# Performance work log

Measured on AMD Instinct MI355X. Metric: run time of the kernel, lower is better.

## Reference

```python
import jax, jax.numpy as jnp
import numpy as np

B, N, K, D = 256, 64, 12, 128


def setup_inputs() -> dict:
    key = jax.random.key(0)
    ks = jax.random.split(key, 12)
    s = 1.0 / np.sqrt(D)
    inp = {
        "nodes_hidden": jax.random.normal(ks[0], (B, N, D), jnp.float32),
        "neighbors_hidden": jax.random.normal(ks[1], (B, N, K, D), jnp.float32),
        # binary neighbor-validity mask (float, as in the torch code)
        "mask": (jax.random.uniform(ks[2], (B, N, K)) < 0.7).astype(jnp.float32),
        "Wq": jax.random.uniform(ks[3], (D, D), jnp.float32, -s, s),
        "bq": jax.random.uniform(ks[4], (D,), jnp.float32, -s, s),
        "Wk": jax.random.uniform(ks[5], (D, D), jnp.float32, -s, s),
        "bk": jax.random.uniform(ks[6], (D,), jnp.float32, -s, s),
        "Wv": jax.random.uniform(ks[7], (D, D), jnp.float32, -s, s),
        "bv": jax.random.uniform(ks[8], (D,), jnp.float32, -s, s),
        # W_att: Linear(2D -> 1); split into the query half and key half of its weight
        "wa_q": jax.random.uniform(ks[9], (D,), jnp.float32, -s, s),
        "wa_k": jax.random.uniform(ks[10], (D,), jnp.float32, -s, s),
        "ba": jax.random.uniform(ks[11], (), jnp.float32, -s, s),
    }
    return inp


def reference(nodes_hidden, neighbors_hidden, mask, Wq, bq, Wk, bk, Wv, bv, wa_q, wa_k, ba):
    # prepend the node itself to its neighbor list: [B,N,K+1,D]
    nh = jnp.concatenate([nodes_hidden[:, :, None, :], neighbors_hidden], axis=2)
    # prepend an always-valid slot to the mask: [B,N,K+1]
    m = jnp.concatenate([jnp.ones(mask.shape[:-1] + (1,), mask.dtype), mask], axis=-1)

    q = nodes_hidden @ Wq + bq            # [B,N,D]
    k = nh @ Wk + bk                      # [B,N,K+1,D]
    v = nh @ Wv + bv                      # [B,N,K+1,D]

    # W_att(cat([q,k])) == q.wa_q + k.wa_k + ba  (avoids materializing the 2D concat)
    sim = (q @ wa_q)[:, :, None] + k @ wa_k + ba   # [B,N,K+1]
    sim = jnp.where(sim >= 0, sim, 0.2 * sim)      # LeakyReLU(0.2)
    sim = jnp.exp(sim) * m                         # masked exp (matches torch exactly)
    attn = sim / (jnp.sum(sim, axis=-1, keepdims=True) + 1e-16)
    return jnp.einsum('bnk,bnkd->bnd', attn, v)    # [B,N,D]
```

## Files before the change

### kernel.cpp

```cpp
#include <hip/hip_runtime.h>


#define B_  256
#define N_  64
#define K_  12
#define D_  128
#define BN  (B_ * N_)
#define ROWS 8
#define NBLK (BN / ROWS)
#define HB_STRIDE 132

__global__ void __launch_bounds__(256)
fused_kernel(const float* __restrict__ nodes, const float* __restrict__ neigh,
             const float* __restrict__ mask,
             const float* __restrict__ Wq, const float* __restrict__ bq,
             const float* __restrict__ Wk, const float* __restrict__ bk,
             const float* __restrict__ Wv, const float* __restrict__ bv,
             const float* __restrict__ wa_q, const float* __restrict__ wa_k,
             const float* __restrict__ ba_p, float* __restrict__ out) {
    __shared__ float weff[256];
    __shared__ float hb[ROWS * HB_STRIDE];
    __shared__ float scL[ROWS];
    __shared__ float cstS;

    const int t    = threadIdx.x;
    const int wave = t >> 6;
    const int l    = t & 63;

    {
        const float*  wrow = (t < 128) ? (Wq + (size_t)t * D_) : (Wk + (size_t)(t - 128) * D_);
        const float*  wa   = (t < 128) ? wa_q : wa_k;
        const float4* wr4  = (const float4*)wrow;
        const float4* wa4  = (const float4*)wa;
        float acc = 0.0f;
        #pragma unroll
        for (int k = 0; k < 32; ++k) {
            float4 a = wr4[k], b = wa4[k];
            acc += a.x * b.x + a.y * b.y + a.z * b.z + a.w * b.w;
        }
        weff[t] = acc;
    }
    if (wave == 0) {
        float2 q2  = ((const float2*)bq)[l];
        float2 k2  = ((const float2*)bk)[l];
        float2 aq2 = ((const float2*)wa_q)[l];
        float2 ak2 = ((const float2*)wa_k)[l];
        float c = q2.x * aq2.x + q2.y * aq2.y + k2.x * ak2.x + k2.y * ak2.y;
        #pragma unroll
        for (int m = 1; m < 64; m <<= 1) c += __shfl_xor(c, m, 64);
        if (l == 0) cstS = c + ba_p[0];
    }
    __syncthreads();

    const float cst = cstS;
    const float2 wqe = ((const float2*)weff)[l];
    const float2 wke = ((const float2*)(weff + 128))[l];

    #pragma unroll
    for (int p = 0; p < 2; ++p) {
        const int lrow = wave * 2 + p;
        const int idx  = blockIdx.x * ROWS + lrow;

        const float2* np = (const float2*)(nodes + (size_t)idx * D_);
        const float2* gp = (const float2*)(neigh + (size_t)idx * K_ * D_);

        float2 x[K_ + 1];
        x[0] = np[l];
        #pragma unroll
        for (int j = 0; j < K_; ++j) x[j + 1] = gp[j * 64 + l];

        float mval = (l < K_) ? mask[(size_t)idx * K_ + l] : 0.0f;

        float pq = x[0].x * wqe.x + x[0].y * wqe.y;
        float pk[K_ + 1];
        #pragma unroll
        for (int j = 0; j <= K_; ++j) pk[j] = x[j].x * wke.x + x[j].y * wke.y;

        #pragma unroll
        for (int m = 1; m < 64; m <<= 1) {
            pq += __shfl_xor(pq, m, 64);
            #pragma unroll
            for (int j = 0; j <= K_; ++j) pk[j] += __shfl_xor(pk[j], m, 64);
        }

        const float base = pq + cst;
        float e[K_ + 1];
        float S = 0.0f;
        #pragma unroll
        for (int j = 0; j <= K_; ++j) {
            float s = base + pk[j];
            s = (s >= 0.0f) ? s : 0.2f * s;
            float mj = (j == 0) ? 1.0f : __shfl(mval, j - 1, 64);
            e[j] = __expf(s) * mj;
            S += e[j];
        }
        const float inv = 1.0f / (S + 1e-16f);

        float h0 = 0.0f, h1 = 0.0f;
        #pragma unroll
        for (int j = 0; j <= K_; ++j) {
            float w = e[j] * inv;
            h0 += w * x[j].x;
            h1 += w * x[j].y;
        }

        *(float2*)(hb + lrow * HB_STRIDE + 2 * l) = make_float2(h0, h1);
        if (l == 0) scL[lrow] = S * inv;
    }
    __syncthreads();

    const int row  = t >> 5;
    const int cg   = t & 31;
    const int row0 = blockIdx.x * ROWS;
    const float4* wv4 = (const float4*)Wv;

    float4 acc = make_float4(0.f, 0.f, 0.f, 0.f);
    #pragma unroll 8
    for (int k = 0; k < D_; ++k) {
        float4 b = wv4[k * 32 + cg];
        float  a = hb[row * HB_STRIDE + k];
        acc.x += a * b.x;
        acc.y += a * b.y;
        acc.z += a * b.z;
        acc.w += a * b.w;
    }

    float4 bvv = ((const float4*)bv)[cg];
    float  s   = scL[row];
    float4 o;
    o.x = acc.x + bvv.x * s;
    o.y = acc.y + bvv.y * s;
    o.z = acc.z + bvv.z * s;
    o.w = acc.w + bvv.w * s;
    *(float4*)(out + (size_t)(row0 + row) * D_ + cg * 4) = o;
}

extern "C" void kernel_launch(void* const* d_in, const int* in_sizes, int n_in,
                              void* d_out, int out_size, void* d_ws, size_t ws_size,
                              hipStream_t stream) {
    const float* nodes = (const float*)d_in[0];
    const float* neigh = (const float*)d_in[1];
    const float* mask  = (const float*)d_in[2];
    const float* Wq    = (const float*)d_in[3];
    const float* bq    = (const float*)d_in[4];
    const float* Wk    = (const float*)d_in[5];
    const float* bk    = (const float*)d_in[6];
    const float* Wv    = (const float*)d_in[7];
    const float* bv    = (const float*)d_in[8];
    const float* wa_q  = (const float*)d_in[9];
    const float* wa_k  = (const float*)d_in[10];
    const float* ba    = (const float*)d_in[11];
    float* out = (float*)d_out;

    fused_kernel<<<NBLK, 256, 0, stream>>>(nodes, neigh, mask, Wq, bq, Wk, bk,
                                           Wv, bv, wa_q, wa_k, ba, out);
}
```

Measured before the change: 224.8 us.

## Double rows per block, software-pipeline row loads, coalesce weff precompute

Each block now handles 16 rows instead of 8, which halves the number of blocks. The per-block Wq/Wk·wa precompute and the Wv reads in the output GEMV are therefore amortized over twice as many rows. Row loads are double-buffered so the next row's neighbor data is fetched while the current row is processed. The weff precompute now uses coalesced float2 reads with wave reductions instead of strided per-thread row reads. The costs are higher register pressure, fewer blocks for occupancy, and 64 serial shuffle reductions per wave in the precompute.

```diff
diff --git a/kernel.cpp b/kernel.cpp
--- a/kernel.cpp
+++ b/kernel.cpp
@@ -6,7 +6,7 @@
 #define K_  12
 #define D_  128
 #define BN  (B_ * N_)
-#define ROWS 8
+#define ROWS 16
 #define NBLK (BN / ROWS)
 #define HB_STRIDE 132
 
@@ -28,17 +28,20 @@
     const int l    = t & 63;
 
     {
-        const float*  wrow = (t < 128) ? (Wq + (size_t)t * D_) : (Wk + (size_t)(t - 128) * D_);
-        const float*  wa   = (t < 128) ? wa_q : wa_k;
-        const float4* wr4  = (const float4*)wrow;
-        const float4* wa4  = (const float4*)wa;
-        float acc = 0.0f;
-        #pragma unroll
-        for (int k = 0; k < 32; ++k) {
-            float4 a = wr4[k], b = wa4[k];
-            acc += a.x * b.x + a.y * b.y + a.z * b.z + a.w * b.w;
+        const bool isQ  = (wave < 2);
+        const float* Wm = isQ ? Wq : Wk;
+        const float* wa = isQ ? wa_q : wa_k;
+        const int base  = (wave & 1) * 64;
+        const int obase = isQ ? 0 : 128;
+        float2 wav = ((const float2*)wa)[l];
+        #pragma unroll 4
+        for (int i = 0; i < 64; ++i) {
+            float2 w2 = ((const float2*)(Wm + (size_t)(base + i) * D_))[l];
+            float p = w2.x * wav.x + w2.y * wav.y;
+            #pragma unroll
+            for (int m = 1; m < 64; m <<= 1) p += __shfl_xor(p, m, 64);
+            if (l == 0) weff[obase + base + i] = p;
         }
-        weff[t] = acc;
     }
     if (wave == 0) {
         float2 q2  = ((const float2*)bq)[l];
@@ -52,87 +55,106 @@
     }
     __syncthreads();
 
-    const float cst = cstS;
+    const float cst  = cstS;
     const float2 wqe = ((const float2*)weff)[l];
     const float2 wke = ((const float2*)(weff + 128))[l];
 
-    #pragma unroll
-    for (int p = 0; p < 2; ++p) {
-        const int lrow = wave * 2 + p;
-        const int idx  = blockIdx.x * ROWS + lrow;
+    float2 xa[K_ + 1], xb[K_ + 1];
+    float ma, mb;
 
-        const float2* np = (const float2*)(nodes + (size_t)idx * D_);
-        const float2* gp = (const float2*)(neigh + (size_t)idx * K_ * D_);
+#define LOADP(X, M, p) do {                                                   \
+        const int idx_ = blockIdx.x * ROWS + wave * 4 + (p);                  \
+        const float2* np_ = (const float2*)(nodes + (size_t)idx_ * D_);       \
+        const float2* gp_ = (const float2*)(neigh + (size_t)idx_ * (K_*D_)); \
+        X[0] = np_[l];                                                        \
+        _Pragma("unroll")                                                     \
+        for (int j = 0; j < K_; ++j) X[j + 1] = gp_[j * 64 + l];              \
+        M = (l < K_) ? mask[(size_t)idx_ * K_ + l] : 0.0f;                    \
+    } while (0)
 
-        float2 x[K_ + 1];
-        x[0] = np[l];
-        #pragma unroll
-        for (int j = 0; j < K_; ++j) x[j + 1] = gp[j * 64 + l];
+#define PROCP(X, M, p) do {                                                   \
+        const int lrow_ = wave * 4 + (p);                                     \
+        float pq = X[0].x * wqe.x + X[0].y * wqe.y;                           \
+        float pk[K_ + 1];                                                     \
+        _Pragma("unroll")                                                     \
+        for (int j = 0; j <= K_; ++j)                                         \
+            pk[j] = X[j].x * wke.x + X[j].y * wke.y;                          \
+        _Pragma("unroll")                                                     \
+        for (int m_ = 1; m_ < 64; m_ <<= 1) {                                 \
+            pq += __shfl_xor(pq, m_, 64);                                     \
+            _Pragma("unroll")                                                 \
+            for (int j = 0; j <= K_; ++j) pk[j] += __shfl_xor(pk[j], m_, 64); \
+        }                                                                     \
+        const float base_ = pq + cst;                                         \
+        float e[K_ + 1];                                                      \
+        float S = 0.0f;                                                       \
+        _Pragma("unroll")                                                     \
+        for (int j = 0; j <= K_; ++j) {                                       \
+            float s_ = base_ + pk[j];                                         \
+            s_ = (s_ >= 0.0f) ? s_ : 0.2f * s_;                               \
+            float mj = (j == 0) ? 1.0f : __shfl(M, j - 1, 64);                \
+            e[j] = __expf(s_) * mj;                                           \
+            S += e[j];                                                        \
+        }                                                                     \
+        const float inv_ = 1.0f / (S + 1e-16f);                               \
+        float h0 = 0.0f, h1 = 0.0f;                                           \
+        _Pragma("unroll")                                                     \
+        for (int j = 0; j <= K_; ++j) {                                       \
+            float w_ = e[j] * inv_;                                           \
+            h0 += w_ * X[j].x;                                                \
+            h1 += w_ * X[j].y;                                                \
+        }                                                                     \
+        *(float2*)(hb + lrow_ * HB_STRIDE + 2 * l) = make_float2(h0, h1);     \
+        if (l == 0) scL[lrow_] = S * inv_;                                    \
+    } while (0)
 
-        float mval = (l < K_) ? mask[(size_t)idx * K_ + l] : 0.0f;
+    LOADP(xa, ma, 0);
+    LOADP(xb, mb, 1);
+    PROCP(xa, ma, 0);
+    LOADP(xa, ma, 2);
+    PROCP(xb, mb, 1);
+    LOADP(xb, mb, 3);
+    PROCP(xa, ma, 2);
+    PROCP(xb, mb, 3);
 
-        float pq = x[0].x * wqe.x + x[0].y * wqe.y;
-        float pk[K_ + 1];
-        #pragma unroll
-        for (int j = 0; j <= K_; ++j) pk[j] = x[j].x * wke.x + x[j].y * wke.y;
+#undef LOADP
+#undef PROCP
 
-        #pragma unroll
-        for (int m = 1; m < 64; m <<= 1) {
-            pq += __shfl_xor(pq, m, 64);
-            #pragma unroll
-            for (int j = 0; j <= K_; ++j) pk[j] += __shfl_xor(pk[j], m, 64);
-        }
-
-        const float base = pq + cst;
-        float e[K_ + 1];
-        float S = 0.0f;
-        #pragma unroll
-        for (int j = 0; j <= K_; ++j) {
-            float s = base + pk[j];
-            s = (s >= 0.0f) ? s : 0.2f * s;
-            float mj = (j == 0) ? 1.0f : __shfl(mval, j - 1, 64);
-            e[j] = __expf(s) * mj;
-            S += e[j];
-        }
-        const float inv = 1.0f / (S + 1e-16f);
-
-        float h0 = 0.0f, h1 = 0.0f;
-        #pragma unroll
-        for (int j = 0; j <= K_; ++j) {
-            float w = e[j] * inv;
-            h0 += w * x[j].x;
-            h1 += w * x[j].y;
-        }
-
-        *(float2*)(hb + lrow * HB_STRIDE + 2 * l) = make_float2(h0, h1);
-        if (l == 0) scL[lrow] = S * inv;
-    }
     __syncthreads();
 
-    const int row  = t >> 5;
+    const int rg   = t >> 5;
     const int cg   = t & 31;
     const int row0 = blockIdx.x * ROWS;
     const float4* wv4 = (const float4*)Wv;
 
-    float4 acc = make_float4(0.f, 0.f, 0.f, 0.f);
+    float4 acc0 = make_float4(0.f, 0.f, 0.f, 0.f);
+    float4 acc1 = make_float4(0.f, 0.f, 0.f, 0.f);
     #pragma unroll 8
     for (int k = 0; k < D_; ++k) {
-        float4 b = wv4[k * 32 + cg];
-        float  a = hb[row * HB_STRIDE + k];
-        acc.x += a * b.x;
-        acc.y += a * b.y;
-        acc.z += a * b.z;
-        acc.w += a * b.w;
+        float4 b  = wv4[k * 32 + cg];
+        float  a0 = hb[rg * HB_STRIDE + k];
+        float  a1 = hb[(rg + 8) * HB_STRIDE + k];
+        acc0.x += a0 * b.x;  acc0.y += a0 * b.y;
+        acc0.z += a0 * b.z;  acc0.w += a0 * b.w;
+        acc1.x += a1 * b.x;  acc1.y += a1 * b.y;
+        acc1.z += a1 * b.z;  acc1.w += a1 * b.w;
     }
 
     float4 bvv = ((const float4*)bv)[cg];
-    float  s   = scL[row];
-    float4 o;
-    o.x = acc.x + bvv.x * s;
-    o.y = acc.y + bvv.y * s;
-    o.z = acc.z + bvv.z * s;
-    o.w = acc.w + bvv.w * s;
-    *(float4*)(out + (size_t)(row0 + row) * D_ + cg * 4) = o;
+    {
+        float s = scL[rg];
+        float4 o;
+        o.x = acc0.x + bvv.x * s;  o.y = acc0.y + bvv.y * s;
+        o.z = acc0.z + bvv.z * s;  o.w = acc0.w + bvv.w * s;
+        *(float4*)(out + (size_t)(row0 + rg) * D_ + cg * 4) = o;
+    }
+    {
+        float s = scL[rg + 8];
+        float4 o;
+        o.x = acc1.x + bvv.x * s;  o.y = acc1.y + bvv.y * s;
+        o.z = acc1.z + bvv.z * s;  o.w = acc1.w + bvv.w * s;
+        *(float4*)(out + (size_t)(row0 + rg + 8) * D_ + cg * 4) = o;
+    }
 }
 
 extern "C" void kernel_launch(void* const* d_in, const int* in_sizes, int n_in,
```

New measurement: 224.6 us. No clear change (-0.1%).

## Double rows per block, half-wave per row with float4 loads, coalesced weff prologue

Applied to the files above, without the earlier changes.

Each block now handles 16 rows instead of 8, and each half-wave processes one row with float4 loads, so the shuffle reductions need 5 steps instead of 6. The mask is broadcast with a ballot instead of per-neighbor shuffles. The Wq/Wk·wa prologue is reorganised so 16 lanes cooperate per row, giving coalesced reads. The Wv GEMV computes two rows per thread so each Wv load is reused twice. This halves the per-block prologue and Wv traffic relative to the rows processed, at the cost of more registers (launch bounds now request 4 blocks) and fewer blocks.

```diff
diff --git a/kernel.cpp b/kernel.cpp
--- a/kernel.cpp
+++ b/kernel.cpp
@@ -6,11 +6,11 @@
 #define K_  12
 #define D_  128
 #define BN  (B_ * N_)
-#define ROWS 8
+#define ROWS 16
 #define NBLK (BN / ROWS)
 #define HB_STRIDE 132
 
-__global__ void __launch_bounds__(256)
+__global__ void __launch_bounds__(256, 4)
 fused_kernel(const float* __restrict__ nodes, const float* __restrict__ neigh,
              const float* __restrict__ mask,
              const float* __restrict__ Wq, const float* __restrict__ bq,
@@ -28,17 +28,28 @@
     const int l    = t & 63;
 
     {
-        const float*  wrow = (t < 128) ? (Wq + (size_t)t * D_) : (Wk + (size_t)(t - 128) * D_);
-        const float*  wa   = (t < 128) ? wa_q : wa_k;
-        const float4* wr4  = (const float4*)wrow;
-        const float4* wa4  = (const float4*)wa;
-        float acc = 0.0f;
-        #pragma unroll
-        for (int k = 0; k < 32; ++k) {
-            float4 a = wr4[k], b = wa4[k];
-            acc += a.x * b.x + a.y * b.y + a.z * b.z + a.w * b.w;
+        const bool  isQ  = (wave < 2);
+        const float* Wm  = isQ ? Wq : Wk;
+        const float* wav = isQ ? wa_q : wa_k;
+        const int sub    = l & 15;
+        const int rquad  = l >> 4;
+        const int rbase  = (wave & 1) * 64;
+        const int obase  = isQ ? 0 : 128;
+        float4 wv0 = ((const float4*)wav)[sub * 2];
+        float4 wv1 = ((const float4*)wav)[sub * 2 + 1];
+        #pragma unroll 4
+        for (int i = 0; i < 16; ++i) {
+            int r = rbase + i * 4 + rquad;
+            const float4* wr = (const float4*)(Wm + (size_t)r * D_);
+            float4 a0 = wr[sub * 2], a1 = wr[sub * 2 + 1];
+            float p = a0.x * wv0.x + a0.y * wv0.y + a0.z * wv0.z + a0.w * wv0.w
+                    + a1.x * wv1.x + a1.y * wv1.y + a1.z * wv1.z + a1.w * wv1.w;
+            p += __shfl_xor(p, 1, 64);
+            p += __shfl_xor(p, 2, 64);
+            p += __shfl_xor(p, 4, 64);
+            p += __shfl_xor(p, 8, 64);
+            if (sub == 0) weff[obase + r] = p;
         }
-        weff[t] = acc;
     }
     if (wave == 0) {
         float2 q2  = ((const float2*)bq)[l];
@@ -53,86 +64,103 @@
     __syncthreads();
 
     const float cst = cstS;
-    const float2 wqe = ((const float2*)weff)[l];
-    const float2 wke = ((const float2*)(weff + 128))[l];
+    const int h = l >> 5;
+    const int s = l & 31;
+    const float4 wqe = ((const float4*)weff)[s];
+    const float4 wke = ((const float4*)(weff + 128))[s];
 
     #pragma unroll
-    for (int p = 0; p < 2; ++p) {
-        const int lrow = wave * 2 + p;
+    for (int i = 0; i < 2; ++i) {
+        const int lrow = wave * 4 + i * 2 + h;
         const int idx  = blockIdx.x * ROWS + lrow;
 
-        const float2* np = (const float2*)(nodes + (size_t)idx * D_);
-        const float2* gp = (const float2*)(neigh + (size_t)idx * K_ * D_);
+        const float4* np = (const float4*)(nodes + (size_t)idx * D_);
+        const float4* gp = (const float4*)(neigh + (size_t)idx * (K_ * D_));
 
-        float2 x[K_ + 1];
-        x[0] = np[l];
+        float4 x[K_ + 1];
+        x[0] = np[s];
         #pragma unroll
-        for (int j = 0; j < K_; ++j) x[j + 1] = gp[j * 64 + l];
+        for (int j = 0; j < K_; ++j) x[j + 1] = gp[j * 32 + s];
 
-        float mval = (l < K_) ? mask[(size_t)idx * K_ + l] : 0.0f;
+        float mval = (s < K_) ? mask[(size_t)idx * K_ + s] : 0.0f;
+        unsigned long long mbits = __ballot(mval > 0.5f);
 
-        float pq = x[0].x * wqe.x + x[0].y * wqe.y;
-        float pk[K_ + 1];
+        float pq = x[0].x * wqe.x + x[0].y * wqe.y + x[0].z * wqe.z + x[0].w * wqe.w;
+        float tj[K_ + 1];
         #pragma unroll
-        for (int j = 0; j <= K_; ++j) pk[j] = x[j].x * wke.x + x[j].y * wke.y;
+        for (int j = 0; j <= K_; ++j)
+            tj[j] = pq + x[j].x * wke.x + x[j].y * wke.y
+                       + x[j].z * wke.z + x[j].w * wke.w;
 
         #pragma unroll
-        for (int m = 1; m < 64; m <<= 1) {
-            pq += __shfl_xor(pq, m, 64);
+        for (int m = 1; m < 32; m <<= 1) {
             #pragma unroll
-            for (int j = 0; j <= K_; ++j) pk[j] += __shfl_xor(pk[j], m, 64);
+            for (int j = 0; j <= K_; ++j) tj[j] += __shfl_xor(tj[j], m, 64);
         }
 
-        const float base = pq + cst;
         float e[K_ + 1];
         float S = 0.0f;
         #pragma unroll
         for (int j = 0; j <= K_; ++j) {
-            float s = base + pk[j];
-            s = (s >= 0.0f) ? s : 0.2f * s;
-            float mj = (j == 0) ? 1.0f : __shfl(mval, j - 1, 64);
-            e[j] = __expf(s) * mj;
+            float sc = tj[j] + cst;
+            sc = (sc >= 0.0f) ? sc : 0.2f * sc;
+            float mj = (j == 0) ? 1.0f
+                     : (((mbits >> (h * 32 + j - 1)) & 1ull) ? 1.0f : 0.0f);
+            e[j] = __expf(sc) * mj;
             S += e[j];
         }
         const float inv = 1.0f / (S + 1e-16f);
 
-        float h0 = 0.0f, h1 = 0.0f;
+        float4 hacc = make_float4(0.f, 0.f, 0.f, 0.f);
         #pragma unroll
         for (int j = 0; j <= K_; ++j) {
             float w = e[j] * inv;
-            h0 += w * x[j].x;
-            h1 += w * x[j].y;
+            hacc.x += w * x[j].x;  hacc.y += w * x[j].y;
+            hacc.z += w * x[j].z;  hacc.w += w * x[j].w;
         }
-
-        *(float2*)(hb + lrow * HB_STRIDE + 2 * l) = make_float2(h0, h1);
-        if (l == 0) scL[lrow] = S * inv;
+        *(float4*)(hb + lrow * HB_STRIDE + s * 4) = hacc;
+        if (s == 0) scL[lrow] = S * inv;
     }
     __syncthreads();
 
-    const int row  = t >> 5;
+    const int rg   = t >> 5;
     const int cg   = t & 31;
     const int row0 = blockIdx.x * ROWS;
     const float4* wv4 = (const float4*)Wv;
 
-    float4 acc = make_float4(0.f, 0.f, 0.f, 0.f);
-    #pragma unroll 8
-    for (int k = 0; k < D_; ++k) {
-        float4 b = wv4[k * 32 + cg];
-        float  a = hb[row * HB_STRIDE + k];
-        acc.x += a * b.x;
-        acc.y += a * b.y;
-        acc.z += a * b.z;
-        acc.w += a * b.w;
+    float4 acc0 = make_float4(0.f, 0.f, 0.f, 0.f);
+    float4 acc1 = make_float4(0.f, 0.f, 0.f, 0.f);
+    #pragma unroll 4
+    for (int k4 = 0; k4 < 32; ++k4) {
+        float4 a0 = *(const float4*)(hb + rg * HB_STRIDE + k4 * 4);
+        float4 a1 = *(const float4*)(hb + (rg + 8) * HB_STRIDE + k4 * 4);
+        #pragma unroll
+        for (int kk = 0; kk < 4; ++kk) {
+            float4 b  = wv4[(k4 * 4 + kk) * 32 + cg];
+            float av0 = (&a0.x)[kk];
+            float av1 = (&a1.x)[kk];
+            acc0.x += av0 * b.x;  acc0.y += av0 * b.y;
+            acc0.z += av0 * b.z;  acc0.w += av0 * b.w;
+            acc1.x += av1 * b.x;  acc1.y += av1 * b.y;
+            acc1.z += av1 * b.z;  acc1.w += av1 * b.w;
+        }
     }
 
     float4 bvv = ((const float4*)bv)[cg];
-    float  s   = scL[row];
-    float4 o;
-    o.x = acc.x + bvv.x * s;
-    o.y = acc.y + bvv.y * s;
-    o.z = acc.z + bvv.z * s;
-    o.w = acc.w + bvv.w * s;
-    *(float4*)(out + (size_t)(row0 + row) * D_ + cg * 4) = o;
+    {
+        float sc = scL[rg];
+        float4 o;
+        o.x = acc0.x + bvv.x * sc;  o.y = acc0.y + bvv.y * sc;
+        o.z = acc0.z + bvv.z * sc;  o.w = acc0.w + bvv.w * sc;
+        *(float4*)(out + (size_t)(row0 + rg) * D_ + cg * 4) = o;
+    }
+    {
+        float sc = scL[rg + 8];
+        float4 o;
+        o.x = acc1.x + bvv.x * sc;  o.y = acc1.y + bvv.y * sc;
+        o.z = acc1.z + bvv.z * sc;  o.w = acc1.w + bvv.w * sc;
+        *(float4*)(out + (size_t)(row0 + rg + 8) * D_ + cg * 4) = o;
+    }
 }
 
 extern "C" void kernel_launch(void* const* d_in, const int* in_sizes, int n_in,
```

New measurement: 203.5 us. 1.1x faster.
